# Kernel tuning notes

Hardware: AMD Instinct MI355X
Metric: run time of the kernel (lower is better)

The kernel has to match this reference:

```python
import jax, jax.numpy as jnp
import numpy as np

NH, DK, W = 16, 64, 128        # n_heads, head_dim, sliding window
D = NH * DK                    # d_model = 1024
NEG = -1.0e9


def setup_inputs() -> dict:
    key = jax.random.key(0)
    k0, k1, k2, k3, k4 = jax.random.split(key, 5)
    L, B, T0 = 128, 8, 4096
    x_chunk = jax.random.normal(k0, (L, B, D), jnp.float32)
    K_cache = jax.random.normal(k1, (T0, B, NH, DK), jnp.float32)
    V_cache = jax.random.normal(k2, (T0, B, NH, DK), jnp.float32)
    s = 1.0 / np.sqrt(D)
    qkv_w = jax.random.normal(k3, (D, 3 * D), jnp.float32) * s
    qkv_b = jnp.zeros((3 * D,), jnp.float32)
    out_w = jax.random.normal(k4, (D, D), jnp.float32) * s
    out_b = jnp.zeros((D,), jnp.float32)
    return {"x_chunk": x_chunk, "K_cache": K_cache, "V_cache": V_cache,
            "qkv_w": qkv_w, "qkv_b": qkv_b, "out_w": out_w, "out_b": out_b}


def reference(x_chunk, K_cache, V_cache, qkv_w, qkv_b, out_w, out_b):
    L, B, Dm = x_chunk.shape
    qkv = (x_chunk @ qkv_w + qkv_b).reshape(L, B, 3, NH, DK)
    q, k, v = qkv[:, :, 0], qkv[:, :, 1], qkv[:, :, 2]
    K = jnp.concatenate([K_cache, k], axis=0)   # [T,B,nh,dk]
    V = jnp.concatenate([V_cache, v], axis=0)
    T = K.shape[0]
    idx = jnp.arange(T)
    # causal mask over global positions (rows = absolute key positions)
    mask = jnp.where(idx[None, :] > idx[:, None], NEG, 0.0)   # [T,T]
    if T > W:  # static shape -> Python if is fine under jit
        valid = jnp.zeros((T,), jnp.float32).at[-W:].set(1.0)
        mask = mask + (1.0 - valid[None, :]) * NEG
    # scores: [B,nh,L,T]
    logits = jnp.einsum('lbhd,tbhd->bhlt', q, K) / np.sqrt(DK)
    logits = logits + mask[-L:, :][None, None]
    weights = jax.nn.softmax(logits, axis=-1)
    o = jnp.einsum('bhlt,tbhd->lbhd', weights, V).reshape(L, B, Dm)
    y = o @ out_w + out_b
    return (y, K, V)
```

## Files before the change

kernel.cpp:

```cpp
#include <hip/hip_runtime.h>

#define L_CHUNK 128
#define BATCH   8
#define NHEADS  16
#define DKDIM   64
#define DMODEL  1024
#define T0CACHE 4096
#define TTOT    4224
#define ROWSTR  8192

#define N8PER   8388608u
#define SPLIT1  5242880u
#define SPLIT2  6815744u

typedef __attribute__((ext_vector_type(8))) __bf16 bf16x8;
typedef __attribute__((ext_vector_type(4))) float f32x4;
typedef __attribute__((ext_vector_type(8))) unsigned short us8;

__device__ __forceinline__ unsigned short f2bf(float f) {
    unsigned int u = __float_as_uint(f);
    u += 0x7fffu + ((u >> 16) & 1u);
    return (unsigned short)(u >> 16);
}

__device__ __forceinline__ void copy_slice(int cid, int ncopy,
        unsigned e0, unsigned e1,
        float4* __restrict__ Kd, const float4* __restrict__ Kc,
        float4* __restrict__ Vd, const float4* __restrict__ Vc) {
    const unsigned stride = (unsigned)ncopy * 256u;
    const unsigned base = e0 + (unsigned)cid * 256u + threadIdx.x;
    for (unsigned e = base; e < e1; e += stride) Kd[e] = Kc[e];
    for (unsigned e = base; e < e1; e += stride) Vd[e] = Vc[e];
}

template<int MODE, bool AF32, bool BF32>
__device__ __forceinline__ void gemm_body(
        int bx, int by,
        const void* __restrict__ Ap,
        const void* __restrict__ Bp,
        const float* __restrict__ bias,
        float* __restrict__ Cf, unsigned short* __restrict__ Cq,
        float* __restrict__ C1, float* __restrict__ C2,
        int K, int N) {
    __shared__ unsigned short Al[64][40];
    __shared__ unsigned short Bl[64][40];

    const int tid  = threadIdx.x;
    const int wave = tid >> 6;
    const int lane = tid & 63;
    const int m0 = by * 64;
    const int n0 = bx * 64;

    f32x4 zero = {0.f, 0.f, 0.f, 0.f};
    f32x4 acc[4];
    #pragma unroll
    for (int i = 0; i < 4; ++i) acc[i] = zero;

    const int ar = tid >> 2, ac = (tid & 3) * 8;
    const int bk = tid >> 3, bn = (tid & 7) * 8;
    const int rot = tid & 7;
    const int mrow = wave * 16 + (lane & 15);
    const int koff = (lane >> 4) * 8;

    for (int k0 = 0; k0 < K; k0 += 32) {
        us8 av, bv;
        if constexpr (AF32) {
            const float* A = (const float*)Ap;
            const float4 a0 = *(const float4*)(A + (size_t)(m0 + ar) * K + (k0 + ac));
            const float4 a1 = *(const float4*)(A + (size_t)(m0 + ar) * K + (k0 + ac) + 4);
            av[0] = f2bf(a0.x); av[1] = f2bf(a0.y); av[2] = f2bf(a0.z); av[3] = f2bf(a0.w);
            av[4] = f2bf(a1.x); av[5] = f2bf(a1.y); av[6] = f2bf(a1.z); av[7] = f2bf(a1.w);
        } else {
            const unsigned short* A = (const unsigned short*)Ap;
            av = *(const us8*)(A + (size_t)(m0 + ar) * K + (k0 + ac));
        }
        if constexpr (BF32) {
            const float* B = (const float*)Bp;
            const float4 b0 = *(const float4*)(B + (size_t)(k0 + bk) * N + (n0 + bn));
            const float4 b1 = *(const float4*)(B + (size_t)(k0 + bk) * N + (n0 + bn) + 4);
            bv[0] = f2bf(b0.x); bv[1] = f2bf(b0.y); bv[2] = f2bf(b0.z); bv[3] = f2bf(b0.w);
            bv[4] = f2bf(b1.x); bv[5] = f2bf(b1.y); bv[6] = f2bf(b1.z); bv[7] = f2bf(b1.w);
        } else {
            const unsigned short* B = (const unsigned short*)Bp;
            bv = *(const us8*)(B + (size_t)(k0 + bk) * N + (n0 + bn));
        }
        *(us8*)(&Al[ar][ac]) = av;
        #pragma unroll
        for (int i = 0; i < 8; ++i) {
            int ii = (i + rot) & 7;
            Bl[bn + ii][bk] = bv[ii];
        }
        __syncthreads();
        bf16x8 af = __builtin_bit_cast(bf16x8, *(const us8*)(&Al[mrow][koff]));
        #pragma unroll
        for (int nt = 0; nt < 4; ++nt) {
            bf16x8 bf = __builtin_bit_cast(bf16x8,
                            *(const us8*)(&Bl[nt * 16 + (lane & 15)][koff]));
            acc[nt] = __builtin_amdgcn_mfma_f32_16x16x32_bf16(af, bf, acc[nt], 0, 0, 0);
        }
        __syncthreads();
    }

    const int colt  = lane & 15;
    const int rbase = (lane >> 4) * 4;
    #pragma unroll
    for (int nt = 0; nt < 4; ++nt) {
        int gcol = n0 + nt * 16 + colt;
        float bval = bias[gcol];
        #pragma unroll
        for (int r = 0; r < 4; ++r) {
            int grow = m0 + wave * 16 + rbase + r;
            float val = acc[nt][r] + bval;
            if (MODE == 0) {
                Cf[(size_t)grow * N + gcol] = val;
            } else {
                int s = gcol >> 10, w = gcol & 1023;
                int l = grow >> 3, b = grow & 7;
                size_t kvoff = (size_t)(T0CACHE + l) * ROWSTR + (size_t)b * DMODEL + w;
                if (s == 0)      Cq[(size_t)grow * DMODEL + w] = f2bf(val);
                else if (s == 1) C1[kvoff] = val;
                else             C2[kvoff] = val;
            }
        }
    }
}

__global__ __launch_bounds__(256) void qkv_and_copy(
        const float* __restrict__ x,
        const float* __restrict__ qkv_w,
        const float* __restrict__ qkv_b,
        unsigned short* __restrict__ qb,
        float* __restrict__ Kout, float* __restrict__ Vout,
        const float4* __restrict__ Kc, const float4* __restrict__ Vc) {
    const int g = blockIdx.x;
    const bool isGemm = (g < 3072) && ((g & 3) == 0);
    if (isGemm) {
        int gi = g >> 2;
        gemm_body<1, true, true>(gi % 48, gi / 48, x, qkv_w, qkv_b,
                                 nullptr, qb, Kout, Vout, DMODEL, 3 * DMODEL);
    } else {
        int cid = (g < 3072) ? (g - (g >> 2) - 1) : (g - 768);
        copy_slice(cid, 2560, 0u, SPLIT1, (float4*)Kout, Kc, (float4*)Vout, Vc);
    }
}

__global__ __launch_bounds__(256) void attn_mfma(
        const unsigned short* __restrict__ qb,
        const float* __restrict__ Kout,
        const float* __restrict__ Vout,
        unsigned short* __restrict__ ob,
        const float4* __restrict__ Kc, const float4* __restrict__ Vc) {
    __shared__ unsigned short Kb[128][72];
    __shared__ unsigned short Vt[64][136];
    __shared__ unsigned short Pb[4][16][136];

    if (blockIdx.x >= 256) {
        copy_slice(blockIdx.x - 256, 768, SPLIT1, SPLIT2,
                   (float4*)Kout, Kc, (float4*)Vout, Vc);
        return;
    }

    const int tid  = threadIdx.x;
    const int wave = tid >> 6, lane = tid & 63;
    const int qh = blockIdx.x & 1, bh = blockIdx.x >> 1;
    const int b = bh >> 4, h = bh & 15;
    const int q0 = qh * 64;
    const size_t base = (size_t)T0CACHE * ROWSTR + (size_t)b * DMODEL + h * DKDIM;

    for (int e = tid; e < 2048; e += 256) {
        int j = e >> 4, d4 = (e & 15) * 4;
        float4 kv = *(const float4*)(Kout + base + (size_t)j * ROWSTR + d4);
        ushort4 u; u.x = f2bf(kv.x); u.y = f2bf(kv.y); u.z = f2bf(kv.z); u.w = f2bf(kv.w);
        *(ushort4*)&Kb[j][d4] = u;
        float4 vv = *(const float4*)(Vout + base + (size_t)j * ROWSTR + d4);
        Vt[d4 + 0][j] = f2bf(vv.x); Vt[d4 + 1][j] = f2bf(vv.y);
        Vt[d4 + 2][j] = f2bf(vv.z); Vt[d4 + 3][j] = f2bf(vv.w);
    }

    const int qrow = q0 + wave * 16 + (lane & 15);
    const size_t arow = (size_t)(qrow * 8 + b) * DMODEL + h * DKDIM;
    bf16x8 qa0 = __builtin_bit_cast(bf16x8, *(const us8*)(qb + arow + (lane >> 4) * 8));
    bf16x8 qa1 = __builtin_bit_cast(bf16x8, *(const us8*)(qb + arow + 32 + (lane >> 4) * 8));
    __syncthreads();

    f32x4 sacc[8];
    f32x4 zero = {0.f, 0.f, 0.f, 0.f};
    #pragma unroll
    for (int t = 0; t < 8; ++t) sacc[t] = zero;
    #pragma unroll
    for (int t = 0; t < 8; ++t) {
        bf16x8 k0 = __builtin_bit_cast(bf16x8,
                        *(const us8*)(&Kb[t * 16 + (lane & 15)][(lane >> 4) * 8]));
        bf16x8 k1 = __builtin_bit_cast(bf16x8,
                        *(const us8*)(&Kb[t * 16 + (lane & 15)][32 + (lane >> 4) * 8]));
        sacc[t] = __builtin_amdgcn_mfma_f32_16x16x32_bf16(qa0, k0, sacc[t], 0, 0, 0);
        sacc[t] = __builtin_amdgcn_mfma_f32_16x16x32_bf16(qa1, k1, sacc[t], 0, 0, 0);
    }

    const int col = lane & 15;
    float mrow[4], lsum[4], inv[4];
    #pragma unroll
    for (int r = 0; r < 4; ++r) mrow[r] = -3e38f;
    #pragma unroll
    for (int t = 0; t < 8; ++t) {
        #pragma unroll
        for (int r = 0; r < 4; ++r) {
            int key = t * 16 + col;
            int qi  = q0 + wave * 16 + (lane >> 4) * 4 + r;
            float v = sacc[t][r] * 0.125f;
            if (key > qi) v = -1e9f;
            sacc[t][r] = v;
            mrow[r] = fmaxf(mrow[r], v);
        }
    }
    #pragma unroll
    for (int r = 0; r < 4; ++r) {
        #pragma unroll
        for (int off = 1; off < 16; off <<= 1)
            mrow[r] = fmaxf(mrow[r], __shfl_xor(mrow[r], off, 64));
        lsum[r] = 0.f;
    }
    #pragma unroll
    for (int t = 0; t < 8; ++t) {
        #pragma unroll
        for (int r = 0; r < 4; ++r) {
            float p = __expf(sacc[t][r] - mrow[r]);
            lsum[r] += p;
            Pb[wave][(lane >> 4) * 4 + r][t * 16 + col] = f2bf(p);
        }
    }
    #pragma unroll
    for (int r = 0; r < 4; ++r) {
        #pragma unroll
        for (int off = 1; off < 16; off <<= 1)
            lsum[r] += __shfl_xor(lsum[r], off, 64);
        inv[r] = 1.f / lsum[r];
    }
    __syncthreads();

    bf16x8 pa[4];
    #pragma unroll
    for (int ks = 0; ks < 4; ++ks)
        pa[ks] = __builtin_bit_cast(bf16x8,
                     *(const us8*)(&Pb[wave][lane & 15][ks * 32 + (lane >> 4) * 8]));
    f32x4 oacc[4];
    #pragma unroll
    for (int n = 0; n < 4; ++n) oacc[n] = zero;
    #pragma unroll
    for (int n = 0; n < 4; ++n) {
        #pragma unroll
        for (int ks = 0; ks < 4; ++ks) {
            bf16x8 vb = __builtin_bit_cast(bf16x8,
                            *(const us8*)(&Vt[n * 16 + (lane & 15)][ks * 32 + (lane >> 4) * 8]));
            oacc[n] = __builtin_amdgcn_mfma_f32_16x16x32_bf16(pa[ks], vb, oacc[n], 0, 0, 0);
        }
    }

    #pragma unroll
    for (int n = 0; n < 4; ++n) {
        #pragma unroll
        for (int r = 0; r < 4; ++r) {
            int qi = q0 + wave * 16 + (lane >> 4) * 4 + r;
            int d  = n * 16 + col;
            ob[(size_t)(qi * 8 + b) * DMODEL + h * DKDIM + d] = f2bf(oacc[n][r] * inv[r]);
        }
    }
}

__global__ __launch_bounds__(256) void out_gemm(
        const unsigned short* __restrict__ ob,
        const float* __restrict__ out_w,
        const float* __restrict__ out_b, float* __restrict__ y,
        float* __restrict__ Kout, float* __restrict__ Vout,
        const float4* __restrict__ Kc, const float4* __restrict__ Vc) {
    const int g = blockIdx.x;
    if (g >= 256) {
        copy_slice(g - 256, 768, SPLIT2, N8PER,
                   (float4*)Kout, Kc, (float4*)Vout, Vc);
        return;
    }
    gemm_body<0, false, true>(g & 15, g >> 4, ob, out_w, out_b,
                              y, nullptr, nullptr, nullptr, DMODEL, DMODEL);
}

extern "C" void kernel_launch(void* const* d_in, const int* in_sizes, int n_in,
                              void* d_out, int out_size, void* d_ws, size_t ws_size,
                              hipStream_t stream) {
    const float* x     = (const float*)d_in[0];
    const float* Kc    = (const float*)d_in[1];
    const float* Vc    = (const float*)d_in[2];
    const float* qkv_w = (const float*)d_in[3];
    const float* qkv_b = (const float*)d_in[4];
    const float* out_w = (const float*)d_in[5];
    const float* out_b = (const float*)d_in[6];

    float* y    = (float*)d_out;
    float* Kout = y + (size_t)L_CHUNK * BATCH * DMODEL;
    float* Vout = Kout + (size_t)TTOT * ROWSTR;

    char* ws = (char*)d_ws;
    unsigned short* qb = (unsigned short*)ws;
    unsigned short* ob = (unsigned short*)(ws + (size_t)(2 << 20));

    qkv_and_copy<<<3328, 256, 0, stream>>>(x, qkv_w, qkv_b, qb, Kout, Vout,
                                           (const float4*)Kc, (const float4*)Vc);

    attn_mfma<<<1024, 256, 0, stream>>>(qb, Kout, Vout, ob,
                                        (const float4*)Kc, (const float4*)Vc);

    out_gemm<<<1024, 256, 0, stream>>>(ob, out_w, out_b, y, Kout, Vout,
                                       (const float4*)Kc, (const float4*)Vc);
}
```

Before: 572.3 us.

## Prefetch GEMM tiles into registers and rebalance cache copy across attention and output kernels

The shared GEMM body now issues the global loads for the next K tile before running MFMA on the current one, a register-level software pipeline that hides load latency. The QKV kernel no longer carries any KV-cache copy blocks. The whole copy is split evenly between the attention and output-GEMM kernels, which each launch 2048 copy blocks, and the copy loops are unrolled by 4. The aim is to keep the small QKV GEMM off the bandwidth-bound copy and overlap the copy with the later stages, at the cost of extra registers and an added barrier per iteration.

```diff
diff --git a/kernel.cpp b/kernel.cpp
--- a/kernel.cpp
+++ b/kernel.cpp
@@ -10,8 +10,7 @@
 #define ROWSTR  8192
 
 #define N8PER   8388608u
-#define SPLIT1  5242880u
-#define SPLIT2  6815744u
+#define CSPLIT  4194304u
 
 typedef __attribute__((ext_vector_type(8))) __bf16 bf16x8;
 typedef __attribute__((ext_vector_type(4))) float f32x4;
@@ -29,7 +28,9 @@
         float4* __restrict__ Vd, const float4* __restrict__ Vc) {
     const unsigned stride = (unsigned)ncopy * 256u;
     const unsigned base = e0 + (unsigned)cid * 256u + threadIdx.x;
+    #pragma unroll 4
     for (unsigned e = base; e < e1; e += stride) Kd[e] = Kc[e];
+    #pragma unroll 4
     for (unsigned e = base; e < e1; e += stride) Vd[e] = Vc[e];
 }
 
@@ -62,35 +63,43 @@
     const int mrow = wave * 16 + (lane & 15);
     const int koff = (lane >> 4) * 8;
 
-    for (int k0 = 0; k0 < K; k0 += 32) {
+    float4 a0, a1, b0, b1;
+    us8 a16, b16;
+
+    auto LOAD = [&](int k0) {
+        if constexpr (AF32) {
+            const float* A = (const float*)Ap;
+            a0 = *(const float4*)(A + (size_t)(m0 + ar) * K + (k0 + ac));
+            a1 = *(const float4*)(A + (size_t)(m0 + ar) * K + (k0 + ac) + 4);
+        } else {
+            a16 = *(const us8*)((const unsigned short*)Ap + (size_t)(m0 + ar) * K + (k0 + ac));
+        }
+        if constexpr (BF32) {
+            const float* B = (const float*)Bp;
+            b0 = *(const float4*)(B + (size_t)(k0 + bk) * N + (n0 + bn));
+            b1 = *(const float4*)(B + (size_t)(k0 + bk) * N + (n0 + bn) + 4);
+        } else {
+            b16 = *(const us8*)((const unsigned short*)Bp + (size_t)(k0 + bk) * N + (n0 + bn));
+        }
+    };
+    auto STORE = [&]() {
         us8 av, bv;
         if constexpr (AF32) {
-            const float* A = (const float*)Ap;
-            const float4 a0 = *(const float4*)(A + (size_t)(m0 + ar) * K + (k0 + ac));
-            const float4 a1 = *(const float4*)(A + (size_t)(m0 + ar) * K + (k0 + ac) + 4);
             av[0] = f2bf(a0.x); av[1] = f2bf(a0.y); av[2] = f2bf(a0.z); av[3] = f2bf(a0.w);
             av[4] = f2bf(a1.x); av[5] = f2bf(a1.y); av[6] = f2bf(a1.z); av[7] = f2bf(a1.w);
-        } else {
-            const unsigned short* A = (const unsigned short*)Ap;
-            av = *(const us8*)(A + (size_t)(m0 + ar) * K + (k0 + ac));
-        }
+        } else av = a16;
         if constexpr (BF32) {
-            const float* B = (const float*)Bp;
-            const float4 b0 = *(const float4*)(B + (size_t)(k0 + bk) * N + (n0 + bn));
-            const float4 b1 = *(const float4*)(B + (size_t)(k0 + bk) * N + (n0 + bn) + 4);
             bv[0] = f2bf(b0.x); bv[1] = f2bf(b0.y); bv[2] = f2bf(b0.z); bv[3] = f2bf(b0.w);
             bv[4] = f2bf(b1.x); bv[5] = f2bf(b1.y); bv[6] = f2bf(b1.z); bv[7] = f2bf(b1.w);
-        } else {
-            const unsigned short* B = (const unsigned short*)Bp;
-            bv = *(const us8*)(B + (size_t)(k0 + bk) * N + (n0 + bn));
-        }
+        } else bv = b16;
         *(us8*)(&Al[ar][ac]) = av;
         #pragma unroll
         for (int i = 0; i < 8; ++i) {
             int ii = (i + rot) & 7;
             Bl[bn + ii][bk] = bv[ii];
         }
-        __syncthreads();
+    };
+    auto COMPUTE = [&]() {
         bf16x8 af = __builtin_bit_cast(bf16x8, *(const us8*)(&Al[mrow][koff]));
         #pragma unroll
         for (int nt = 0; nt < 4; ++nt) {
@@ -98,8 +107,19 @@
                             *(const us8*)(&Bl[nt * 16 + (lane & 15)][koff]));
             acc[nt] = __builtin_amdgcn_mfma_f32_16x16x32_bf16(af, bf, acc[nt], 0, 0, 0);
         }
+    };
+
+    LOAD(0);
+    STORE();
+    __syncthreads();
+    for (int k0 = 32; k0 < K; k0 += 32) {
+        LOAD(k0);
+        COMPUTE();
         __syncthreads();
-    }
+        STORE();
+        __syncthreads();
+    }
+    COMPUTE();
 
     const int colt  = lane & 15;
     const int rbase = (lane >> 4) * 4;
@@ -125,23 +145,15 @@
     }
 }
 
-__global__ __launch_bounds__(256) void qkv_and_copy(
+__global__ __launch_bounds__(256) void qkv_gemm(
         const float* __restrict__ x,
         const float* __restrict__ qkv_w,
         const float* __restrict__ qkv_b,
         unsigned short* __restrict__ qb,
-        float* __restrict__ Kout, float* __restrict__ Vout,
-        const float4* __restrict__ Kc, const float4* __restrict__ Vc) {
-    const int g = blockIdx.x;
-    const bool isGemm = (g < 3072) && ((g & 3) == 0);
-    if (isGemm) {
-        int gi = g >> 2;
-        gemm_body<1, true, true>(gi % 48, gi / 48, x, qkv_w, qkv_b,
-                                 nullptr, qb, Kout, Vout, DMODEL, 3 * DMODEL);
-    } else {
-        int cid = (g < 3072) ? (g - (g >> 2) - 1) : (g - 768);
-        copy_slice(cid, 2560, 0u, SPLIT1, (float4*)Kout, Kc, (float4*)Vout, Vc);
-    }
+        float* __restrict__ Kout, float* __restrict__ Vout) {
+    int gi = blockIdx.x;
+    gemm_body<1, true, true>(gi % 48, gi / 48, x, qkv_w, qkv_b,
+                             nullptr, qb, Kout, Vout, DMODEL, 3 * DMODEL);
 }
 
 __global__ __launch_bounds__(256) void attn_mfma(
@@ -155,7 +167,7 @@
     __shared__ unsigned short Pb[4][16][136];
 
     if (blockIdx.x >= 256) {
-        copy_slice(blockIdx.x - 256, 768, SPLIT1, SPLIT2,
+        copy_slice(blockIdx.x - 256, 2048, 0u, CSPLIT,
                    (float4*)Kout, Kc, (float4*)Vout, Vc);
         return;
     }
@@ -275,7 +287,7 @@
         const float4* __restrict__ Kc, const float4* __restrict__ Vc) {
     const int g = blockIdx.x;
     if (g >= 256) {
-        copy_slice(g - 256, 768, SPLIT2, N8PER,
+        copy_slice(g - 256, 2048, CSPLIT, N8PER,
                    (float4*)Kout, Kc, (float4*)Vout, Vc);
         return;
     }
@@ -302,12 +314,11 @@
     unsigned short* qb = (unsigned short*)ws;
     unsigned short* ob = (unsigned short*)(ws + (size_t)(2 << 20));
 
-    qkv_and_copy<<<3328, 256, 0, stream>>>(x, qkv_w, qkv_b, qb, Kout, Vout,
-                                           (const float4*)Kc, (const float4*)Vc);
-
-    attn_mfma<<<1024, 256, 0, stream>>>(qb, Kout, Vout, ob,
+    qkv_gemm<<<768, 256, 0, stream>>>(x, qkv_w, qkv_b, qb, Kout, Vout);
+
+    attn_mfma<<<2304, 256, 0, stream>>>(qb, Kout, Vout, ob,
                                         (const float4*)Kc, (const float4*)Vc);
 
-    out_gemm<<<1024, 256, 0, stream>>>(ob, out_w, out_b, y, Kout, Vout,
+    out_gemm<<<2304, 256, 0, stream>>>(ob, out_w, out_b, y, Kout, Vout,
                                        (const float4*)Kc, (const float4*)Vc);
 }
```

After: 542.5 us. 5.2% less time.
